# Kernel tuning notes

Hardware: AMD Instinct MI355X
Metric: run time of the kernel (lower is better)

Reference implementation:

```python
import jax, jax.numpy as jnp
import numpy as np

N_NODES = 100000
N_EDGES = 1600000
IN_DIM = 128
OUT_DIM = 128


def setup_inputs() -> dict:
    key = jax.random.key(0)
    k1, k2, k3, k4, k5 = jax.random.split(key, 5)
    x = jax.random.normal(k1, (N_NODES, IN_DIM), dtype=jnp.float32)
    edge_index = jax.random.randint(k2, (2, N_EDGES), 0, N_NODES, dtype=jnp.int64)
    s = 1.0 / np.sqrt(IN_DIM)
    # PyG SAGEConv params: lin_l (neighbor branch, with bias), lin_r (root branch, no bias)
    W_l = jax.random.uniform(k3, (OUT_DIM, IN_DIM), jnp.float32, -s, s)
    b_l = jax.random.uniform(k4, (OUT_DIM,), jnp.float32, -s, s)
    W_r = jax.random.uniform(k5, (OUT_DIM, IN_DIM), jnp.float32, -s, s)
    return {"x": x, "edge_index": edge_index, "W_l": W_l, "b_l": b_l, "W_r": W_r}


def reference(x, edge_index, W_l, b_l, W_r):
    src = edge_index[0]  # message source j
    dst = edge_index[1]  # aggregation target i
    # mean aggregation of neighbor features at each target node
    msg_sum = jax.ops.segment_sum(x[src], dst, num_segments=N_NODES)  # [N, in]
    deg = jax.ops.segment_sum(jnp.ones((N_EDGES,), x.dtype), dst, num_segments=N_NODES)
    agg = msg_sum / jnp.maximum(deg, 1.0)[:, None]
    # out = lin_l(agg) + lin_r(x)
    out = agg @ W_l.T + b_l + x @ W_r.T  # [N, out]
    # L2 normalize (F.normalize, p=2, dim=-1, eps=1e-12)
    norm = jnp.sqrt(jnp.sum(out * out, axis=-1, keepdims=True))
    out = out / jnp.maximum(norm, 1e-12)
    return out
```

## Files before the change

### kernel.cpp

```cpp
#include <hip/hip_runtime.h>
#include <hip/hip_fp16.h>
#include <stdint.h>

#define NN 100000
#define D 128
#define W0 128
#define NB ((NN + W0 - 1) / W0)
#define C1 8192

typedef _Float16 f16x8 __attribute__((ext_vector_type(8)));
typedef float f32x4 __attribute__((ext_vector_type(4)));

static const size_t O_FLAG   = 0;
static const size_t O_BCNT   = 256;
static const size_t O_BSTART = O_BCNT + 4096;
static const size_t O_BCUR   = O_BSTART + 4096;
static const size_t O_WTL    = O_BCUR + 4096;
static const size_t O_WTR    = O_WTL + (size_t)D * D * 4;
static const size_t O_OFFS   = O_WTR + (size_t)D * D * 4;
static const size_t O_DEG    = O_OFFS + (size_t)(NN + 64) * 4;
static const size_t O_RECS   = O_DEG + (size_t)NN * 4;

__global__ void k_detect(const int* __restrict__ ei, int* flag) {
    if (threadIdx.x == 0 && blockIdx.x == 0) {
        int ok = 1;
        for (int j = 0; j < 128; ++j)
            if (ei[2 * j + 1] != 0) { ok = 0; break; }
        *flag = ok;
    }
}

__device__ __forceinline__ int edge_at(const int* ei, long long pos, int is64) {
    return is64 ? ei[2 * pos] : ei[pos];
}

__global__ void k_transpose(const float* __restrict__ Wl, const float* __restrict__ Wr,
                            float* __restrict__ WtL, float* __restrict__ WtR) {
    int t = blockIdx.x * 256 + threadIdx.x;
    if (t < D * D) {
        int o = t >> 7, k = t & 127;
        WtL[k * D + o] = Wl[t];
        WtR[k * D + o] = Wr[t];
    }
}

__global__ __launch_bounds__(256) void k_pack(const float* __restrict__ Wl,
                                              const float* __restrict__ Wr,
                                              __half* __restrict__ Bp) {
    int idx = blockIdx.x * 256 + threadIdx.x;
    if (idx >= 32768) return;
    int j  = idx & 7;
    int l  = (idx >> 3) & 63;
    int tt = (idx >> 9) & 7;
    int s  = idx >> 12;
    int col = tt * 16 + (l & 15);
    int k   = s * 32 + (l >> 4) * 8 + j;
    float v = (k < 128) ? Wl[col * 128 + k] : Wr[col * 128 + (k - 128)];
    Bp[idx] = __float2half_rn(v);
}

__global__ __launch_bounds__(256) void k_conv(const float* __restrict__ x,
                                              __half* __restrict__ xh, long long n4) {
    long long i = (long long)blockIdx.x * 256 + threadIdx.x;
    if (i >= n4) return;
    float4 v = ((const float4*)x)[i];
    __half2 h0 = __floats2half2_rn(v.x, v.y);
    __half2 h1 = __floats2half2_rn(v.z, v.w);
    ((__half2*)xh)[2 * i]     = h0;
    ((__half2*)xh)[2 * i + 1] = h1;
}

__global__ __launch_bounds__(256) void k_p1count(const int* __restrict__ ei,
                                                 const int* __restrict__ flag,
                                                 int* __restrict__ bcount, long long E) {
    __shared__ int cnt[NB];
    for (int i = threadIdx.x; i < NB; i += 256) cnt[i] = 0;
    __syncthreads();
    int is64 = *flag;
    long long base = (long long)blockIdx.x * C1;
    for (int j = threadIdx.x; j < C1; j += 256) {
        long long e = base + j;
        if (e < E) {
            int d = edge_at(ei, E + e, is64);
            atomicAdd(&cnt[d >> 7], 1);
        }
    }
    __syncthreads();
    for (int i = threadIdx.x; i < NB; i += 256) {
        int c = cnt[i];
        if (c) atomicAdd(&bcount[i], c);
    }
}

__global__ __launch_bounds__(1024) void k_bscan(const int* __restrict__ bcount,
                                                int* __restrict__ bstart,
                                                int* __restrict__ bcur,
                                                int* __restrict__ offs) {
    __shared__ int sh[1024];
    int t = threadIdx.x;
    sh[t] = (t < NB) ? bcount[t] : 0;
    __syncthreads();
    for (int d = 1; d < 1024; d <<= 1) {
        int v = (t >= d) ? sh[t - d] : 0;
        __syncthreads();
        sh[t] += v;
        __syncthreads();
    }
    if (t < NB) {
        int ex = (t > 0) ? sh[t - 1] : 0;
        bstart[t] = ex;
        bcur[t] = ex;
    }
    if (t == NB - 1) {
        bstart[NB] = sh[NB - 1];
        offs[NN] = sh[NB - 1];
    }
}

__global__ __launch_bounds__(256) void k_p1scatter(const int* __restrict__ ei,
                                                   const int* __restrict__ flag,
                                                   int* __restrict__ bcur,
                                                   unsigned int* __restrict__ recs,
                                                   long long E) {
    __shared__ int cnt[NB];
    __shared__ int rbase[NB];
    for (int i = threadIdx.x; i < NB; i += 256) cnt[i] = 0;
    __syncthreads();
    int is64 = *flag;
    long long base = (long long)blockIdx.x * C1;
    for (int j = threadIdx.x; j < C1; j += 256) {
        long long e = base + j;
        if (e < E) {
            int d = edge_at(ei, E + e, is64);
            atomicAdd(&cnt[d >> 7], 1);
        }
    }
    __syncthreads();
    for (int i = threadIdx.x; i < NB; i += 256) {
        int c = cnt[i];
        rbase[i] = c ? atomicAdd(&bcur[i], c) : 0;
    }
    __syncthreads();
    for (int i = threadIdx.x; i < NB; i += 256) cnt[i] = 0;
    __syncthreads();
    for (int j = threadIdx.x; j < C1; j += 256) {
        long long e = base + j;
        if (e < E) {
            int s = edge_at(ei, e, is64);
            int d = edge_at(ei, E + e, is64);
            int bu = d >> 7;
            int pos = rbase[bu] + atomicAdd(&cnt[bu], 1);
            recs[pos] = (unsigned)s | ((unsigned)(d & (W0 - 1)) << 20);
        }
    }
}

__global__ __launch_bounds__(256) void k_p2(const unsigned int* __restrict__ recs,
                                            const int* __restrict__ bstart,
                                            int* __restrict__ offs,
                                            int* __restrict__ srcs, int N) {
    __shared__ int cnt[W0];
    __shared__ int off[W0];
    int t = threadIdx.x;
    int bu = blockIdx.x;
    int e0 = bstart[bu], e1 = bstart[bu + 1];
    if (t < W0) cnt[t] = 0;
    __syncthreads();
    for (int e = e0 + t; e < e1; e += 256)
        atomicAdd(&cnt[recs[e] >> 20], 1);
    __syncthreads();
    if (t < W0) off[t] = cnt[t];
    __syncthreads();
    for (int d = 1; d < W0; d <<= 1) {
        int v = 0;
        if (t < W0 && t >= d) v = off[t - d];
        __syncthreads();
        if (t < W0) off[t] += v;
        __syncthreads();
    }
    if (t < W0) {
        int ex = (t > 0) ? off[t - 1] : 0;
        int node = bu * W0 + t;
        if (node < N) offs[node] = e0 + ex;
        cnt[t] = e0 + ex;
    }
    __syncthreads();
    for (int e = e0 + t; e < e1; e += 256) {
        unsigned r = recs[e];
        int pos = atomicAdd(&cnt[r >> 20], 1);
        srcs[pos] = (int)(r & 0xFFFFFu);
    }
}

__global__ __launch_bounds__(256) void k_agg_hh(const __half* __restrict__ xh,
                                                const int* __restrict__ offs,
                                                const int* __restrict__ srcs,
                                                __half* agg, int N) {
    int lane = threadIdx.x & 63;
    int wid = __builtin_amdgcn_readfirstlane(threadIdx.x >> 6);
    int node = blockIdx.x * 4 + wid;
    if (node >= N) return;
    int e0 = offs[node], e1 = offs[node + 1];
    const __half2* x2 = (const __half2*)xh;
    float ax = 0.f, ay = 0.f;
    int e = e0;
    for (; e + 4 <= e1; e += 4) {
        int s0 = srcs[e], s1 = srcs[e + 1], s2 = srcs[e + 2], s3 = srcs[e + 3];
        __half2 h0 = x2[(long long)s0 * 64 + lane];
        __half2 h1 = x2[(long long)s1 * 64 + lane];
        __half2 h2 = x2[(long long)s2 * 64 + lane];
        __half2 h3 = x2[(long long)s3 * 64 + lane];
        float2 v0 = __half22float2(h0);
        float2 v1 = __half22float2(h1);
        float2 v2 = __half22float2(h2);
        float2 v3 = __half22float2(h3);
        ax += v0.x + v1.x + v2.x + v3.x;
        ay += v0.y + v1.y + v2.y + v3.y;
    }
    for (; e < e1; ++e) {
        int s = srcs[e];
        float2 v = __half22float2(x2[(long long)s * 64 + lane]);
        ax += v.x; ay += v.y;
    }
    float inv = 1.0f / fmaxf((float)(e1 - e0), 1.0f);
    ((__half2*)agg)[(long long)node * 64 + lane] = __floats2half2_rn(ax * inv, ay * inv);
}

__global__ __launch_bounds__(256) void k_agg_h(const __half* __restrict__ xh,
                                               const int* __restrict__ offs,
                                               const int* __restrict__ srcs,
                                               float* agg, int N) {
    int lane = threadIdx.x & 63;
    int wid = __builtin_amdgcn_readfirstlane(threadIdx.x >> 6);
    int node = blockIdx.x * 4 + wid;
    if (node >= N) return;
    int e0 = offs[node], e1 = offs[node + 1];
    const __half2* x2 = (const __half2*)xh;
    float ax = 0.f, ay = 0.f;
    int e = e0;
    for (; e + 4 <= e1; e += 4) {
        int s0 = srcs[e], s1 = srcs[e + 1], s2 = srcs[e + 2], s3 = srcs[e + 3];
        __half2 h0 = x2[(long long)s0 * 64 + lane];
        __half2 h1 = x2[(long long)s1 * 64 + lane];
        __half2 h2 = x2[(long long)s2 * 64 + lane];
        __half2 h3 = x2[(long long)s3 * 64 + lane];
        float2 v0 = __half22float2(h0);
        float2 v1 = __half22float2(h1);
        float2 v2 = __half22float2(h2);
        float2 v3 = __half22float2(h3);
        ax += v0.x + v1.x + v2.x + v3.x;
        ay += v0.y + v1.y + v2.y + v3.y;
    }
    for (; e < e1; ++e) {
        int s = srcs[e];
        float2 v = __half22float2(x2[(long long)s * 64 + lane]);
        ax += v.x; ay += v.y;
    }
    float inv = 1.0f / fmaxf((float)(e1 - e0), 1.0f);
    float2 o; o.x = ax * inv; o.y = ay * inv;
    ((float2*)agg)[(long long)node * 64 + lane] = o;
}

__global__ __launch_bounds__(256) void k_agg(const float* __restrict__ x,
                                             const int* __restrict__ offs,
                                             const int* __restrict__ srcs,
                                             float* agg, int N) {
    int lane = threadIdx.x & 63;
    int wid = __builtin_amdgcn_readfirstlane(threadIdx.x >> 6);
    int node = blockIdx.x * 4 + wid;
    if (node >= N) return;
    int e0 = offs[node], e1 = offs[node + 1];
    const float2* x2 = (const float2*)x;
    float ax = 0.f, ay = 0.f;
    int e = e0;
    for (; e + 4 <= e1; e += 4) {
        int s0 = srcs[e], s1 = srcs[e + 1], s2 = srcs[e + 2], s3 = srcs[e + 3];
        float2 v0 = x2[(long long)s0 * 64 + lane];
        float2 v1 = x2[(long long)s1 * 64 + lane];
        float2 v2 = x2[(long long)s2 * 64 + lane];
        float2 v3 = x2[(long long)s3 * 64 + lane];
        ax += v0.x + v1.x + v2.x + v3.x;
        ay += v0.y + v1.y + v2.y + v3.y;
    }
    for (; e < e1; ++e) {
        int s = srcs[e];
        float2 v = x2[(long long)s * 64 + lane];
        ax += v.x; ay += v.y;
    }
    float inv = 1.0f / fmaxf((float)(e1 - e0), 1.0f);
    float2 o; o.x = ax * inv; o.y = ay * inv;
    ((float2*)agg)[(long long)node * 64 + lane] = o;
}

__global__ __launch_bounds__(256) void k_scatterB(const float* __restrict__ x,
                                                  const int* __restrict__ ei,
                                                  const int* __restrict__ flag,
                                                  float* out, float* deg, long long E) {
    int lane = threadIdx.x & 63;
    long long e = (long long)blockIdx.x * 4 + (threadIdx.x >> 6);
    if (e >= E) return;
    int is64 = *flag;
    int s = edge_at(ei, e, is64);
    int d = edge_at(ei, E + e, is64);
    atomicAdd(&out[(long long)d * D + lane], x[(long long)s * D + lane]);
    atomicAdd(&out[(long long)d * D + 64 + lane], x[(long long)s * D + 64 + lane]);
    if (lane == 0) atomicAdd(&deg[d], 1.0f);
}

__global__ void k_meanB(float* out, const float* __restrict__ deg) {
    long long i = (long long)blockIdx.x * 256 + threadIdx.x;
    if (i >= (long long)NN * D) return;
    out[i] *= 1.0f / fmaxf(deg[i >> 7], 1.0f);
}

__global__ __launch_bounds__(256) void k_gemm_m(const __half* __restrict__ aggh,
                                                const __half* __restrict__ xh,
                                                const __half* __restrict__ Bp,
                                                const float* __restrict__ bl,
                                                float* __restrict__ out, int N) {
    __shared__ __half Bs[32768];
    int t = threadIdx.x;
#pragma unroll
    for (int i = 0; i < 16; ++i) {
        int idx = t + i * 256;
        ((float4*)Bs)[idx] = ((const float4*)Bp)[idx];
    }
    int lane = t & 63;
    int wid  = t >> 6;
    int row0 = blockIdx.x * 128 + wid * 32;
    int rA = row0 + (lane & 15);
    int rB = rA + 16;
    long long ra = (rA < N) ? rA : (N - 1);
    long long rb = (rB < N) ? rB : (N - 1);
    int koff = (lane >> 4) * 8;

    f32x4 acc[2][8];
#pragma unroll
    for (int r = 0; r < 2; ++r)
#pragma unroll
        for (int c = 0; c < 8; ++c)
            acc[r][c] = (f32x4){0.f, 0.f, 0.f, 0.f};

    __syncthreads();

#pragma unroll
    for (int s = 0; s < 8; ++s) {
        const __half* Ap = (s < 4) ? aggh : xh;
        int kb = (s & 3) * 32 + koff;
        f16x8 a0 = *(const f16x8*)(Ap + ra * 128 + kb);
        f16x8 a1 = *(const f16x8*)(Ap + rb * 128 + kb);
        const __half* bs = Bs + s * 4096 + lane * 8;
#pragma unroll
        for (int tt = 0; tt < 8; ++tt) {
            f16x8 b = *(const f16x8*)(bs + tt * 512);
            acc[0][tt] = __builtin_amdgcn_mfma_f32_16x16x32_f16(a0, b, acc[0][tt], 0, 0, 0);
            acc[1][tt] = __builtin_amdgcn_mfma_f32_16x16x32_f16(a1, b, acc[1][tt], 0, 0, 0);
        }
    }

    float bias[8];
#pragma unroll
    for (int tt = 0; tt < 8; ++tt) bias[tt] = bl[tt * 16 + (lane & 15)];

#pragma unroll
    for (int rt = 0; rt < 2; ++rt) {
#pragma unroll
        for (int r = 0; r < 4; ++r) {
            int row = row0 + rt * 16 + (lane >> 4) * 4 + r;
            float v[8];
            float ss = 0.f;
#pragma unroll
            for (int tt = 0; tt < 8; ++tt) {
                v[tt] = acc[rt][tt][r] + bias[tt];
                ss = fmaf(v[tt], v[tt], ss);
            }
            ss += __shfl_xor(ss, 1, 64);
            ss += __shfl_xor(ss, 2, 64);
            ss += __shfl_xor(ss, 4, 64);
            ss += __shfl_xor(ss, 8, 64);
            float scale = 1.0f / fmaxf(sqrtf(ss), 1e-12f);
            if (row < N) {
                float* op = out + (long long)row * D + (lane & 15);
#pragma unroll
                for (int tt = 0; tt < 8; ++tt)
                    op[tt * 16] = v[tt] * scale;
            }
        }
    }
}

__global__ __launch_bounds__(256) void k_gemm(const float* __restrict__ x,
                                              const float* agg,
                                              const float* __restrict__ WtL,
                                              const float* __restrict__ WtR,
                                              const float* __restrict__ bl,
                                              float* out, int N) {
    __shared__ float Bs[64 * D];
    int t = threadIdx.x;
    int tx = t & 15;
    int ty = t >> 4;
    int row0 = blockIdx.x * 64 + ty * 4;
    int c0a = tx * 4;
    int c0b = 64 + tx * 4;

    float acc[4][8];
    float4 b0 = *(const float4*)(bl + c0a);
    float4 b1 = *(const float4*)(bl + c0b);
#pragma unroll
    for (int r = 0; r < 4; ++r) {
        acc[r][0] = b0.x; acc[r][1] = b0.y; acc[r][2] = b0.z; acc[r][3] = b0.w;
        acc[r][4] = b1.x; acc[r][5] = b1.y; acc[r][6] = b1.z; acc[r][7] = b1.w;
    }

    long long rws[4];
#pragma unroll
    for (int r = 0; r < 4; ++r) {
        int rr = row0 + r;
        rws[r] = (rr < N) ? (long long)rr : (long long)(N - 1);
    }

    for (int phase = 0; phase < 2; ++phase) {
        const float* A = phase ? x : agg;
        const float* W = phase ? WtR : WtL;
        const float4* Ar0 = (const float4*)(A + rws[0] * D);
        const float4* Ar1 = (const float4*)(A + rws[1] * D);
        const float4* Ar2 = (const float4*)(A + rws[2] * D);
        const float4* Ar3 = (const float4*)(A + rws[3] * D);

        for (int half = 0; half < 2; ++half) {
            if (phase | half) __syncthreads();
#pragma unroll
            for (int i = 0; i < 8; ++i) {
                int idx = t + i * 256;
                ((float4*)Bs)[idx] = ((const float4*)(W + half * 64 * D))[idx];
            }
            __syncthreads();

#pragma unroll 2
            for (int k4 = 0; k4 < 16; ++k4) {
                int ak4 = half * 16 + k4;
                float4 av[4];
                av[0] = Ar0[ak4]; av[1] = Ar1[ak4]; av[2] = Ar2[ak4]; av[3] = Ar3[ak4];
#pragma unroll
                for (int kk = 0; kk < 4; ++kk) {
                    int k = k4 * 4 + kk;
                    float4 w0 = *(const float4*)&Bs[k * D + c0a];
                    float4 w1 = *(const float4*)&Bs[k * D + c0b];
#pragma unroll
                    for (int r = 0; r < 4; ++r) {
                        float a = (kk == 0) ? av[r].x : (kk == 1) ? av[r].y
                                 : (kk == 2) ? av[r].z : av[r].w;
                        acc[r][0] = fmaf(a, w0.x, acc[r][0]);
                        acc[r][1] = fmaf(a, w0.y, acc[r][1]);
                        acc[r][2] = fmaf(a, w0.z, acc[r][2]);
                        acc[r][3] = fmaf(a, w0.w, acc[r][3]);
                        acc[r][4] = fmaf(a, w1.x, acc[r][4]);
                        acc[r][5] = fmaf(a, w1.y, acc[r][5]);
                        acc[r][6] = fmaf(a, w1.z, acc[r][6]);
                        acc[r][7] = fmaf(a, w1.w, acc[r][7]);
                    }
                }
            }
        }
    }

#pragma unroll
    for (int r = 0; r < 4; ++r) {
        float s = 0.f;
#pragma unroll
        for (int j = 0; j < 8; ++j) s = fmaf(acc[r][j], acc[r][j], s);
        s += __shfl_xor(s, 1, 64);
        s += __shfl_xor(s, 2, 64);
        s += __shfl_xor(s, 4, 64);
        s += __shfl_xor(s, 8, 64);
        float scale = 1.0f / fmaxf(sqrtf(s), 1e-12f);
        int rr = row0 + r;
        if (rr < N) {
            float4 v0, v1;
            v0.x = acc[r][0] * scale; v0.y = acc[r][1] * scale;
            v0.z = acc[r][2] * scale; v0.w = acc[r][3] * scale;
            v1.x = acc[r][4] * scale; v1.y = acc[r][5] * scale;
            v1.z = acc[r][6] * scale; v1.w = acc[r][7] * scale;
            float* op = out + (long long)rr * D;
            *(float4*)(op + c0a) = v0;
            *(float4*)(op + c0b) = v1;
        }
    }
}

extern "C" void kernel_launch(void* const* d_in, const int* in_sizes, int n_in,
                              void* d_out, int out_size, void* d_ws, size_t ws_size,
                              hipStream_t stream) {
    const float* x  = (const float*)d_in[0];
    const int*   ei = (const int*)d_in[1];
    const float* Wl = (const float*)d_in[2];
    const float* bl = (const float*)d_in[3];
    const float* Wr = (const float*)d_in[4];
    float* out = (float*)d_out;
    const long long E = (long long)in_sizes[1] / 2;

    char* ws = (char*)d_ws;
    int*      flag   = (int*)(ws + O_FLAG);
    int*      bcount = (int*)(ws + O_BCNT);
    int*      bstart = (int*)(ws + O_BSTART);
    int*      bcur   = (int*)(ws + O_BCUR);
    float*    WtL    = (float*)(ws + O_WTL);
    float*    WtR    = (float*)(ws + O_WTR);
    __half*   Bph    = (__half*)(ws + O_WTL);
    int*      offs   = (int*)(ws + O_OFFS);
    float*    deg    = (float*)(ws + O_DEG);
    unsigned* recs   = (unsigned*)(ws + O_RECS);
    int*      srcs   = (int*)(ws + O_RECS + (size_t)E * 4);
    const size_t O_XH = O_RECS + (size_t)E * 8;
    __half*   xh     = (__half*)(ws + O_XH);
    const size_t O_AGGH = O_XH + (size_t)NN * D * 2;
    __half*   aggh   = (__half*)(ws + O_AGGH);

    size_t planA_bytes = O_RECS + (size_t)E * 8;
    size_t fp16_bytes  = O_XH + (size_t)NN * D * 2;
    size_t mfma_bytes  = O_AGGH + (size_t)NN * D * 2;
    bool planA = ws_size >= planA_bytes;
    bool useH  = ws_size >= fp16_bytes;
    bool useM  = planA && (ws_size >= mfma_bytes);

    k_detect<<<1, 64, 0, stream>>>(ei, flag);
    if (useM)
        k_pack<<<128, 256, 0, stream>>>(Wl, Wr, Bph);
    else
        k_transpose<<<(D * D + 255) / 256, 256, 0, stream>>>(Wl, Wr, WtL, WtR);

    if (planA) {
        int pblocks = (int)((E + C1 - 1) / C1);
        hipMemsetAsync(ws + O_BCNT, 0, (size_t)NB * 4, stream);
        if (useH) {
            long long n4 = (long long)NN * D / 4;
            k_conv<<<(int)((n4 + 255) / 256), 256, 0, stream>>>(x, xh, n4);
        }
        k_p1count<<<pblocks, 256, 0, stream>>>(ei, flag, bcount, E);
        k_bscan<<<1, 1024, 0, stream>>>(bcount, bstart, bcur, offs);
        k_p1scatter<<<pblocks, 256, 0, stream>>>(ei, flag, bcur, recs, E);
        k_p2<<<NB, 256, 0, stream>>>(recs, bstart, offs, srcs, NN);
        if (useM) {
            k_agg_hh<<<(NN + 3) / 4, 256, 0, stream>>>(xh, offs, srcs, aggh, NN);
            k_gemm_m<<<(NN + 127) / 128, 256, 0, stream>>>(aggh, xh, Bph, bl, out, NN);
            return;
        }
        if (useH)
            k_agg_h<<<(NN + 3) / 4, 256, 0, stream>>>(xh, offs, srcs, out, NN);
        else
            k_agg<<<(NN + 3) / 4, 256, 0, stream>>>(x, offs, srcs, out, NN);
    } else {
        hipMemsetAsync(out, 0, (size_t)NN * D * 4, stream);
        hipMemsetAsync(ws + O_DEG, 0, (size_t)NN * 4, stream);
        k_scatterB<<<(int)((E + 3) / 4), 256, 0, stream>>>(x, ei, flag, out, deg, E);
        k_meanB<<<(int)(((long long)NN * D + 255) / 256), 256, 0, stream>>>(out, deg);
    }
    k_gemm<<<(NN + 63) / 64, 256, 0, stream>>>(x, out, WtL, WtR, bl, out, NN);
}
```

Measured before the change: 259.2 us.

## Reuse per-block bucket histograms in scatter, vectorize fp16 aggregation, parallelize detect

The count pass now stores each block's bucket histogram, so the scatter pass can reserve its output ranges up front instead of recounting. The edge chunk size per block is halved. The fp16 neighbour aggregation now has four edge groups per wavefront, each loading 16-byte fp16x8 vectors, with partial sums combined by cross-lane shuffles. This targets gather memory-level parallelism. The dtype-detection kernel now uses a wave ballot instead of a serial loop. Together these add workspace for the histograms and more shuffle work per node.

```diff
diff --git a/kernel.cpp b/kernel.cpp
--- a/kernel.cpp
+++ b/kernel.cpp
@@ -6,7 +6,7 @@
 #define D 128
 #define W0 128
 #define NB ((NN + W0 - 1) / W0)
-#define C1 8192
+#define C1 4096
 
 typedef _Float16 f16x8 __attribute__((ext_vector_type(8)));
 typedef float f32x4 __attribute__((ext_vector_type(4)));
@@ -21,13 +21,13 @@
 static const size_t O_DEG    = O_OFFS + (size_t)(NN + 64) * 4;
 static const size_t O_RECS   = O_DEG + (size_t)NN * 4;
 
-__global__ void k_detect(const int* __restrict__ ei, int* flag) {
-    if (threadIdx.x == 0 && blockIdx.x == 0) {
-        int ok = 1;
-        for (int j = 0; j < 128; ++j)
-            if (ei[2 * j + 1] != 0) { ok = 0; break; }
-        *flag = ok;
-    }
+__global__ void k_detect(const int* __restrict__ ei, int* flag, long long E) {
+    int l = threadIdx.x;
+    int bad = 0;
+    if (l < E)       bad |= (ei[2 * l + 1] != 0);
+    if (l + 64 < E)  bad |= (ei[2 * (l + 64) + 1] != 0);
+    unsigned long long m = __ballot(bad);
+    if (l == 0) *flag = (m == 0ull) ? 1 : 0;
 }
 
 __device__ __forceinline__ int edge_at(const int* ei, long long pos, int is64) {
@@ -72,7 +72,8 @@
 
 __global__ __launch_bounds__(256) void k_p1count(const int* __restrict__ ei,
                                                  const int* __restrict__ flag,
-                                                 int* __restrict__ bcount, long long E) {
+                                                 int* __restrict__ bcount,
+                                                 int* __restrict__ bhist, long long E) {
     __shared__ int cnt[NB];
     for (int i = threadIdx.x; i < NB; i += 256) cnt[i] = 0;
     __syncthreads();
@@ -88,6 +89,7 @@
     __syncthreads();
     for (int i = threadIdx.x; i < NB; i += 256) {
         int c = cnt[i];
+        if (bhist) bhist[(long long)blockIdx.x * NB + i] = c;
         if (c) atomicAdd(&bcount[i], c);
     }
 }
@@ -114,6 +116,36 @@
     if (t == NB - 1) {
         bstart[NB] = sh[NB - 1];
         offs[NN] = sh[NB - 1];
+    }
+}
+
+__global__ __launch_bounds__(256) void k_p1scatter2(const int* __restrict__ ei,
+                                                    const int* __restrict__ flag,
+                                                    int* __restrict__ bcur,
+                                                    const int* __restrict__ bhist,
+                                                    unsigned int* __restrict__ recs,
+                                                    long long E) {
+    __shared__ int cnt[NB];
+    __shared__ int rbase[NB];
+    int t = threadIdx.x;
+    const int* h = bhist + (long long)blockIdx.x * NB;
+    for (int i = t; i < NB; i += 256) {
+        int c = h[i];
+        rbase[i] = c ? atomicAdd(&bcur[i], c) : 0;
+        cnt[i] = 0;
+    }
+    __syncthreads();
+    int is64 = *flag;
+    long long base = (long long)blockIdx.x * C1;
+    for (int j = t; j < C1; j += 256) {
+        long long e = base + j;
+        if (e < E) {
+            int s = edge_at(ei, e, is64);
+            int d = edge_at(ei, E + e, is64);
+            int bu = d >> 7;
+            int pos = rbase[bu] + atomicAdd(&cnt[bu], 1);
+            recs[pos] = (unsigned)s | ((unsigned)(d & (W0 - 1)) << 20);
+        }
     }
 }
 
@@ -192,38 +224,41 @@
     }
 }
 
-__global__ __launch_bounds__(256) void k_agg_hh(const __half* __restrict__ xh,
-                                                const int* __restrict__ offs,
-                                                const int* __restrict__ srcs,
-                                                __half* agg, int N) {
+__global__ __launch_bounds__(256) void k_agg_hh4(const __half* __restrict__ xh,
+                                                 const int* __restrict__ offs,
+                                                 const int* __restrict__ srcs,
+                                                 __half* __restrict__ agg, int N) {
     int lane = threadIdx.x & 63;
-    int wid = __builtin_amdgcn_readfirstlane(threadIdx.x >> 6);
+    int wid  = __builtin_amdgcn_readfirstlane(threadIdx.x >> 6);
     int node = blockIdx.x * 4 + wid;
     if (node >= N) return;
     int e0 = offs[node], e1 = offs[node + 1];
-    const __half2* x2 = (const __half2*)xh;
-    float ax = 0.f, ay = 0.f;
-    int e = e0;
-    for (; e + 4 <= e1; e += 4) {
-        int s0 = srcs[e], s1 = srcs[e + 1], s2 = srcs[e + 2], s3 = srcs[e + 3];
-        __half2 h0 = x2[(long long)s0 * 64 + lane];
-        __half2 h1 = x2[(long long)s1 * 64 + lane];
-        __half2 h2 = x2[(long long)s2 * 64 + lane];
-        __half2 h3 = x2[(long long)s3 * 64 + lane];
-        float2 v0 = __half22float2(h0);
-        float2 v1 = __half22float2(h1);
-        float2 v2 = __half22float2(h2);
-        float2 v3 = __half22float2(h3);
-        ax += v0.x + v1.x + v2.x + v3.x;
-        ay += v0.y + v1.y + v2.y + v3.y;
-    }
-    for (; e < e1; ++e) {
-        int s = srcs[e];
-        float2 v = __half22float2(x2[(long long)s * 64 + lane]);
-        ax += v.x; ay += v.y;
-    }
-    float inv = 1.0f / fmaxf((float)(e1 - e0), 1.0f);
-    ((__half2*)agg)[(long long)node * 64 + lane] = __floats2half2_rn(ax * inv, ay * inv);
+    int grp = lane >> 4;
+    int li  = lane & 15;
+    float acc[8] = {0.f, 0.f, 0.f, 0.f, 0.f, 0.f, 0.f, 0.f};
+    for (int e = e0; e < e1; e += 4) {
+        int ee = e + grp;
+        bool ok = ee < e1;
+        int s = srcs[ok ? ee : e0];
+        f16x8 v = *(const f16x8*)(xh + (long long)s * 128 + li * 8);
+        if (ok) {
+#pragma unroll
+            for (int j = 0; j < 8; ++j) acc[j] += (float)v[j];
+        }
+    }
+#pragma unroll
+    for (int j = 0; j < 8; ++j) {
+        acc[j] += __shfl_xor(acc[j], 16, 64);
+        acc[j] += __shfl_xor(acc[j], 32, 64);
+    }
+    if (grp == 0) {
+        float inv = 1.0f / fmaxf((float)(e1 - e0), 1.0f);
+        __half2 o[4];
+#pragma unroll
+        for (int j = 0; j < 4; ++j)
+            o[j] = __floats2half2_rn(acc[2 * j] * inv, acc[2 * j + 1] * inv);
+        *(float4*)(agg + (long long)node * 128 + li * 8) = *(float4*)o;
+    }
 }
 
 __global__ __launch_bounds__(256) void k_agg_h(const __half* __restrict__ xh,
@@ -240,14 +275,10 @@
     int e = e0;
     for (; e + 4 <= e1; e += 4) {
         int s0 = srcs[e], s1 = srcs[e + 1], s2 = srcs[e + 2], s3 = srcs[e + 3];
-        __half2 h0 = x2[(long long)s0 * 64 + lane];
-        __half2 h1 = x2[(long long)s1 * 64 + lane];
-        __half2 h2 = x2[(long long)s2 * 64 + lane];
-        __half2 h3 = x2[(long long)s3 * 64 + lane];
-        float2 v0 = __half22float2(h0);
-        float2 v1 = __half22float2(h1);
-        float2 v2 = __half22float2(h2);
-        float2 v3 = __half22float2(h3);
+        float2 v0 = __half22float2(x2[(long long)s0 * 64 + lane]);
+        float2 v1 = __half22float2(x2[(long long)s1 * 64 + lane]);
+        float2 v2 = __half22float2(x2[(long long)s2 * 64 + lane]);
+        float2 v3 = __half22float2(x2[(long long)s3 * 64 + lane]);
         ax += v0.x + v1.x + v2.x + v3.x;
         ay += v0.y + v1.y + v2.y + v3.y;
     }
@@ -515,33 +546,41 @@
     __half*   xh     = (__half*)(ws + O_XH);
     const size_t O_AGGH = O_XH + (size_t)NN * D * 2;
     __half*   aggh   = (__half*)(ws + O_AGGH);
-
-    size_t planA_bytes = O_RECS + (size_t)E * 8;
-    size_t fp16_bytes  = O_XH + (size_t)NN * D * 2;
-    size_t mfma_bytes  = O_AGGH + (size_t)NN * D * 2;
-    bool planA = ws_size >= planA_bytes;
-    bool useH  = ws_size >= fp16_bytes;
-    bool useM  = planA && (ws_size >= mfma_bytes);
-
-    k_detect<<<1, 64, 0, stream>>>(ei, flag);
+    const size_t O_BHIST = O_AGGH + (size_t)NN * D * 2;
+    int*      bhist  = (int*)(ws + O_BHIST);
+
+    int pblocks = (int)((E + C1 - 1) / C1);
+    size_t planA_bytes  = O_RECS + (size_t)E * 8;
+    size_t fp16_bytes   = O_XH + (size_t)NN * D * 2;
+    size_t mfma_bytes   = O_AGGH + (size_t)NN * D * 2;
+    size_t merged_bytes = O_BHIST + (size_t)pblocks * NB * 4;
+    bool planA    = ws_size >= planA_bytes;
+    bool useH     = ws_size >= fp16_bytes;
+    bool useM     = planA && (ws_size >= mfma_bytes);
+    bool useMerge = useM && (ws_size >= merged_bytes);
+
+    k_detect<<<1, 64, 0, stream>>>(ei, flag, E);
     if (useM)
         k_pack<<<128, 256, 0, stream>>>(Wl, Wr, Bph);
     else
         k_transpose<<<(D * D + 255) / 256, 256, 0, stream>>>(Wl, Wr, WtL, WtR);
 
     if (planA) {
-        int pblocks = (int)((E + C1 - 1) / C1);
         hipMemsetAsync(ws + O_BCNT, 0, (size_t)NB * 4, stream);
         if (useH) {
             long long n4 = (long long)NN * D / 4;
             k_conv<<<(int)((n4 + 255) / 256), 256, 0, stream>>>(x, xh, n4);
         }
-        k_p1count<<<pblocks, 256, 0, stream>>>(ei, flag, bcount, E);
+        k_p1count<<<pblocks, 256, 0, stream>>>(ei, flag, bcount,
+                                               useMerge ? bhist : (int*)nullptr, E);
         k_bscan<<<1, 1024, 0, stream>>>(bcount, bstart, bcur, offs);
-        k_p1scatter<<<pblocks, 256, 0, stream>>>(ei, flag, bcur, recs, E);
+        if (useMerge)
+            k_p1scatter2<<<pblocks, 256, 0, stream>>>(ei, flag, bcur, bhist, recs, E);
+        else
+            k_p1scatter<<<pblocks, 256, 0, stream>>>(ei, flag, bcur, recs, E);
         k_p2<<<NB, 256, 0, stream>>>(recs, bstart, offs, srcs, NN);
         if (useM) {
-            k_agg_hh<<<(NN + 3) / 4, 256, 0, stream>>>(xh, offs, srcs, aggh, NN);
+            k_agg_hh4<<<(NN + 3) / 4, 256, 0, stream>>>(xh, offs, srcs, aggh, NN);
             k_gemm_m<<<(NN + 127) / 128, 256, 0, stream>>>(aggh, xh, Bph, bl, out, NN);
             return;
         }
```

After: 266.7 us. 2.9% more time.
